# Performance work log

Hardware: AMD Instinct MI355X
Metric: run time of the kernel (lower is better)

Reference implementation:

```python
import jax, jax.numpy as jnp
import numpy as np

U = 359347   # user_num (hardcoded in source)
I = 292589   # item_num (hardcoded in source)
D = 64       # factor_num
NNZ = 4_000_000
B = 32768
LAM = 0.001  # lamada


def setup_inputs() -> dict:
    key = jax.random.key(0)
    ks = jax.random.split(key, 19)
    return {
        "ui_rows": jax.random.randint(ks[0], (NNZ,), 0, U, dtype=jnp.int32),
        "ui_cols": jax.random.randint(ks[1], (NNZ,), 0, I, dtype=jnp.int32),
        "ui_vals": jax.random.uniform(ks[2], (NNZ,), dtype=jnp.float32),
        "iu_vals": jax.random.uniform(ks[3], (NNZ,), dtype=jnp.float32),
        "d_i": jax.random.uniform(ks[4], (U,), dtype=jnp.float32),
        "d_j": jax.random.uniform(ks[5], (I,), dtype=jnp.float32),
        "embed_user": jax.random.normal(ks[6], (U, D), dtype=jnp.float32) * 0.01,
        "embed_item": jax.random.normal(ks[7], (I, D), dtype=jnp.float32) * 0.01,
        "add_w": jax.random.normal(ks[8], (1, 3), dtype=jnp.float32),
        "fw1": jax.random.normal(ks[9], (2 * D, D), dtype=jnp.float32) * (1.0 / np.sqrt(D)),
        "fb1": jax.random.normal(ks[10], (2 * D,), dtype=jnp.float32) * 0.01,
        "fw2": jax.random.normal(ks[11], (D, 2 * D), dtype=jnp.float32) * (1.0 / np.sqrt(2 * D)),
        "fb2": jax.random.normal(ks[12], (D,), dtype=jnp.float32) * 0.01,
        "user_bias": jax.random.normal(ks[13], (U, 1), dtype=jnp.float32) * 0.01,
        "item_bias": jax.random.normal(ks[14], (I, 1), dtype=jnp.float32) * 0.01,
        "avg_rating": jax.random.uniform(ks[15], (1,), dtype=jnp.float32) * 5.0,
        "user0": jax.random.randint(ks[16], (B,), 0, U, dtype=jnp.int32),
        "item_i0": jax.random.randint(ks[17], (B,), 0, I, dtype=jnp.int32),
        "ratings": jax.random.uniform(ks[18], (B,), dtype=jnp.float32) * 5.0,
    }


def _spmm(rows, cols, vals, x, num_rows):
    # sparse [num_rows, *] COO @ dense x : gather rows of x by col index,
    # scale by edge value, scatter-add into destination rows.
    return jax.ops.segment_sum(vals[:, None] * x[cols], rows, num_segments=num_rows)


def _leaky(x):
    return jnp.where(x > 0, x, 0.1 * x)


def _user_filter(x, fw1, fb1, fw2, fb2):
    h = _leaky(x @ fw1.T + fb1)
    return _leaky(h @ fw2.T + fb2)


def reference(ui_rows, ui_cols, ui_vals, iu_vals, d_i, d_j,
              embed_user, embed_item, add_w, fw1, fb1, fw2, fb2,
              user_bias, item_bias, avg_rating, user0, item_i0, ratings):
    ue, ie = embed_user, embed_item
    # layer 1: SpMM + degree-scaled residual + ReLU
    g1_u = jax.nn.relu(_spmm(ui_rows, ui_cols, ui_vals, ie, U) + ue * d_i[:, None])
    g1_i = jax.nn.relu(_spmm(ui_cols, ui_rows, iu_vals, ue, I) + ie * d_j[:, None])
    # layer 2
    g2_u = jax.nn.relu(_spmm(ui_rows, ui_cols, ui_vals, g1_i, U) + g1_u * d_i[:, None])
    g2_i = jax.nn.relu(_spmm(ui_cols, ui_rows, iu_vals, g1_u, I) + g1_i * d_j[:, None])
    # learned combination of the 3 layers: Linear(3,1) over the stacked axis
    w = add_w[0]  # [3]
    gcn_u = w[0] * ue + w[1] * g1_u + w[2] * g2_u   # [U, D]
    gcn_i = w[0] * ie + w[1] * g1_i + w[2] * g2_i   # [I, D]
    # batch lookup + shared filter MLP
    user = _user_filter(gcn_u[user0], fw1, fb1, fw2, fb2)      # [B, D]
    item = _user_filter(gcn_i[item_i0], fw1, fb1, fw2, fb2)    # [B, D]
    pred = (user * item).sum(-1) + user_bias[user0, 0] + item_bias[item_i0, 0] + avg_rating
    l2 = LAM * jnp.mean(gcn_u ** 2) + LAM * jnp.mean(gcn_i ** 2)
    loss2 = jnp.mean((pred - ratings) ** 2)
    return loss2 + l2
```

## Files before the change

kernel.cpp:

```cpp
#include <hip/hip_runtime.h>

#define U_NUM 359347
#define I_NUM 292589
#define DDIM  64
#define NNZ_N 4000000
#define BATCH 32768
#define LAM_F 0.001f
#define ACC_SLOTS 2048

#define EPB   4096
#define NBLK  ((NNZ_N + EPB - 1) / EPB)
#define NB_U  ((U_NUM + 1023) >> 10)
#define NB_I  ((I_NUM + 1023) >> 10)

__device__ __forceinline__ float leaky(float x) { return x > 0.f ? x : 0.1f * x; }

__device__ __forceinline__ unsigned short f2bf(float f) {
    unsigned b = __float_as_uint(f);
    b = (b + 0x7FFF + ((b >> 16) & 1)) >> 16;
    return (unsigned short)b;
}
__device__ __forceinline__ float bf2f(unsigned short u) {
    return __uint_as_float((unsigned)u << 16);
}
__device__ __forceinline__ float bflo(unsigned u) { return __uint_as_float(u << 16); }
__device__ __forceinline__ float bfhi(unsigned u) { return __uint_as_float(u & 0xffff0000u); }

__device__ __forceinline__ unsigned char f2fp8(float v) {
    v = fminf(fmaxf(v * 64.f, -440.f), 440.f);
    unsigned b = __float_as_uint(v * 0x1p-120f);
    unsigned sign = (b >> 24) & 0x80u;
    unsigned mag = b & 0x7fffffffu;
    mag += 0x7ffffu + ((mag >> 20) & 1u);
    return (unsigned char)(sign | ((mag >> 20) & 0x7fu));
}
#if __has_builtin(__builtin_amdgcn_cvt_f32_fp8)
#define FP8DEC(b) __builtin_amdgcn_cvt_f32_fp8((int)(b), 0)
#else
#define FP8DEC(b) (__uint_as_float(((unsigned)((b) & 0x80u) << 24) | \
                                   ((unsigned)((b) & 0x7fu) << 20)) * 0x1p120f)
#endif

__global__ __launch_bounds__(256) void f2bf8_k(
    const float4* __restrict__ inU, ushort4* __restrict__ obU, uchar4* __restrict__ o8U,
    const float4* __restrict__ inI, ushort4* __restrict__ obI, uchar4* __restrict__ o8I,
    size_t nU4, size_t total4)
{
    size_t stride = (size_t)gridDim.x * 256;
    for (size_t i = (size_t)blockIdx.x * 256 + threadIdx.x; i < total4; i += stride) {
        const float4* in; ushort4* ob; uchar4* o8; size_t j;
        if (i < nU4) { in = inU; ob = obU; o8 = o8U; j = i; }
        else         { in = inI; ob = obI; o8 = o8I; j = i - nU4; }
        float4 v = in[j];
        ushort4 o;
        o.x = f2bf(v.x); o.y = f2bf(v.y); o.z = f2bf(v.z); o.w = f2bf(v.w);
        ob[j] = o;
        uchar4 p;
        p.x = f2fp8(v.x); p.y = f2fp8(v.y); p.z = f2fp8(v.z); p.w = f2fp8(v.w);
        o8[j] = p;
    }
}

__global__ __launch_bounds__(256) void hist2_k(
    const int* __restrict__ rows, const int* __restrict__ cols,
    int* __restrict__ gh_u, int* __restrict__ gh_i)
{
    __shared__ int h[512];
    int sideB = blockIdx.x >= NBLK;
    int blk = sideB ? blockIdx.x - NBLK : blockIdx.x;
    const int* keys = sideB ? cols : rows;
    int nb = sideB ? NB_I : NB_U;
    int* gh = sideB ? gh_i : gh_u;
    for (int i = threadIdx.x; i < nb; i += 256) h[i] = 0;
    __syncthreads();
    int base = blk * EPB;
    int end = min(base + EPB, NNZ_N);
    for (int e = base + threadIdx.x; e < end; e += 256)
        atomicAdd(&h[keys[e] >> 10], 1);
    __syncthreads();
    for (int i = threadIdx.x; i < nb; i += 256)
        gh[i * NBLK + blk] = h[i];
}

__global__ __launch_bounds__(256) void scan1m_k(
    int* __restrict__ aU, int nUe, int* __restrict__ bsU, int nb1U,
    int* __restrict__ aI, int nIe, int* __restrict__ bsI)
{
    __shared__ int s[256];
    int sideB = (int)blockIdx.x >= nb1U;
    int blk = sideB ? blockIdx.x - nb1U : blockIdx.x;
    int* a = sideB ? aI : aU;
    int n = sideB ? nIe : nUe;
    int* bsum = sideB ? bsI : bsU;
    int t = threadIdx.x;
    int base = blk * 1024 + t * 4;
    int v[4];
#pragma unroll
    for (int j = 0; j < 4; ++j) v[j] = (base + j < n) ? a[base + j] : 0;
    s[t] = v[0] + v[1] + v[2] + v[3];
    __syncthreads();
    for (int off = 1; off < 256; off <<= 1) {
        int x = (t >= off) ? s[t - off] : 0;
        __syncthreads();
        s[t] += x;
        __syncthreads();
    }
    if (t == 255) bsum[blk] = s[255];
    int run = (t > 0) ? s[t - 1] : 0;
#pragma unroll
    for (int j = 0; j < 4; ++j) {
        if (base + j < n) a[base + j] = run;
        run += v[j];
    }
}

__global__ __launch_bounds__(512) void scan2m_k(
    int* __restrict__ bsU, int nbU, int* __restrict__ bsI, int nbI)
{
    __shared__ int s[512];
    int* bsum = blockIdx.x ? bsI : bsU;
    int nb = blockIdx.x ? nbI : nbU;
    int t = threadIdx.x;
    int v = (t < nb) ? bsum[t] : 0;
    s[t] = v;
    __syncthreads();
    for (int off = 1; off < 512; off <<= 1) {
        int x = (t >= off) ? s[t - off] : 0;
        __syncthreads();
        s[t] += x;
        __syncthreads();
    }
    if (t < nb) bsum[t] = s[t] - v;
}

__global__ __launch_bounds__(256) void scan3m_k(
    int* __restrict__ aU, int nUe, const int* __restrict__ bsU, int nb1U,
    int* __restrict__ aI, int nIe, const int* __restrict__ bsI)
{
    int sideB = (int)blockIdx.x >= nb1U;
    int blk = sideB ? blockIdx.x - nb1U : blockIdx.x;
    int* a = sideB ? aI : aU;
    int n = sideB ? nIe : nUe;
    int add = (sideB ? bsI : bsU)[blk];
    int base = blk * 1024 + threadIdx.x * 4;
#pragma unroll
    for (int j = 0; j < 4; ++j)
        if (base + j < n) a[base + j] += add;
}

__global__ __launch_bounds__(256) void scat_k(
    const int* __restrict__ keys, const int* __restrict__ cols,
    const float* __restrict__ vals, const int* __restrict__ gh, int nb,
    int2* __restrict__ tmpb, unsigned short* __restrict__ tmpv)
{
    __shared__ int cur[512];
    for (int i = threadIdx.x; i < nb; i += 256) cur[i] = gh[i * NBLK + blockIdx.x];
    __syncthreads();
    int base = blockIdx.x * EPB;
    int end = min(base + EPB, NNZ_N);
    for (int e = base + threadIdx.x; e < end; e += 256) {
        int k = keys[e];
        int pos = atomicAdd(&cur[k >> 10], 1);
        tmpb[pos] = make_int2(k, cols[e]);
        tmpv[pos] = f2bf(vals[e] * 0.015625f);
    }
}

__global__ __launch_bounds__(256) void l2sort_k(
    const int2* __restrict__ tmpb, const unsigned short* __restrict__ tmpv,
    const int* __restrict__ gh, int nb, int* __restrict__ ptr, int nrows,
    int* __restrict__ ecol, unsigned short* __restrict__ eval)
{
    __shared__ int hist[1024];
    __shared__ int ssc[256];
    int b = blockIdx.x;
    int t = threadIdx.x;
    int bucket_base = gh[b * NBLK];
    int bucket_end  = (b == nb - 1) ? NNZ_N : gh[(b + 1) * NBLK];
    for (int i = t; i < 1024; i += 256) hist[i] = 0;
    __syncthreads();
    for (int e = bucket_base + t; e < bucket_end; e += 256)
        atomicAdd(&hist[tmpb[e].x & 1023], 1);
    __syncthreads();
    int v0 = hist[t * 4], v1 = hist[t * 4 + 1], v2 = hist[t * 4 + 2], v3 = hist[t * 4 + 3];
    ssc[t] = v0 + v1 + v2 + v3;
    __syncthreads();
    for (int off = 1; off < 256; off <<= 1) {
        int x = (t >= off) ? ssc[t - off] : 0;
        __syncthreads();
        ssc[t] += x;
        __syncthreads();
    }
    int run = (t > 0) ? ssc[t - 1] : 0;
    int g0 = run, g1 = run + v0, g2 = g1 + v1, g3 = g2 + v2;
    hist[t * 4] = g0; hist[t * 4 + 1] = g1; hist[t * 4 + 2] = g2; hist[t * 4 + 3] = g3;
    int rbase = b << 10;
    if (rbase + t * 4 < nrows)     ptr[rbase + t * 4]     = bucket_base + g0;
    if (rbase + t * 4 + 1 < nrows) ptr[rbase + t * 4 + 1] = bucket_base + g1;
    if (rbase + t * 4 + 2 < nrows) ptr[rbase + t * 4 + 2] = bucket_base + g2;
    if (rbase + t * 4 + 3 < nrows) ptr[rbase + t * 4 + 3] = bucket_base + g3;
    if (b == nb - 1 && t == 0) ptr[nrows] = NNZ_N;
    __syncthreads();
    for (int e = bucket_base + t; e < bucket_end; e += 256) {
        int2 q = tmpb[e];
        int pos = bucket_base + atomicAdd(&hist[q.x & 1023], 1);
        ecol[pos] = q.y;
        eval[pos] = tmpv[e];
    }
}

template <int MODE>
__global__ __launch_bounds__(256) void spmm_dual_k(
    int gA,
    const int* __restrict__ ptrA, const int* __restrict__ ecolA, const unsigned short* __restrict__ evalA,
    const unsigned char* __restrict__ x8A, const unsigned short* baseA, const float* __restrict__ degA,
    unsigned short* outA, int nA, unsigned char* __restrict__ out8A,
    const unsigned short* embedA, float* __restrict__ accA,
    const int* __restrict__ ptrB, const int* __restrict__ ecolB, const unsigned short* __restrict__ evalB,
    const unsigned char* __restrict__ x8B, const unsigned short* baseB, const float* __restrict__ degB,
    unsigned short* outB, int nB, unsigned char* __restrict__ out8B,
    const unsigned short* embedB, float* __restrict__ accB,
    const float* __restrict__ add_w)
{
    int wv = threadIdx.x >> 6, lane = threadIdx.x & 63;
    int bid = blockIdx.x;
    int sideB = bid >= gA;
    int lb = sideB ? bid - gA : bid;
    const int* ptr = sideB ? ptrB : ptrA;
    const int* ecol = sideB ? ecolB : ecolA;
    const unsigned short* eval = sideB ? evalB : evalA;
    const unsigned char* x8 = sideB ? x8B : x8A;
    const unsigned short* base = sideB ? baseB : baseA;
    const float* deg = sideB ? degB : degA;
    unsigned short* out = sideB ? outB : outA;
    int nrows = sideB ? nB : nA;
    __shared__ float ssum[4];
    int r = lb * 4 + wv;
    if (r < nrows) {
        int s0 = __builtin_amdgcn_readfirstlane(ptr[r]);
        int e0 = __builtin_amdgcn_readfirstlane(ptr[r + 1]);
        float a0 = 0.f, a1 = 0.f, a2 = 0.f, a3 = 0.f;
        int k = s0;
        for (; k + 8 <= e0; k += 8) {
            int c0 = ecol[k],     c1 = ecol[k + 1], c2 = ecol[k + 2], c3 = ecol[k + 3];
            int c4 = ecol[k + 4], c5 = ecol[k + 5], c6 = ecol[k + 6], c7 = ecol[k + 7];
            unsigned char b0 = x8[(size_t)c0 * DDIM + lane];
            unsigned char b1 = x8[(size_t)c1 * DDIM + lane];
            unsigned char b2 = x8[(size_t)c2 * DDIM + lane];
            unsigned char b3 = x8[(size_t)c3 * DDIM + lane];
            unsigned char b4 = x8[(size_t)c4 * DDIM + lane];
            unsigned char b5 = x8[(size_t)c5 * DDIM + lane];
            unsigned char b6 = x8[(size_t)c6 * DDIM + lane];
            unsigned char b7 = x8[(size_t)c7 * DDIM + lane];
            a0 = fmaf(bf2f(eval[k]),     FP8DEC(b0), a0);
            a1 = fmaf(bf2f(eval[k + 1]), FP8DEC(b1), a1);
            a2 = fmaf(bf2f(eval[k + 2]), FP8DEC(b2), a2);
            a3 = fmaf(bf2f(eval[k + 3]), FP8DEC(b3), a3);
            a0 = fmaf(bf2f(eval[k + 4]), FP8DEC(b4), a0);
            a1 = fmaf(bf2f(eval[k + 5]), FP8DEC(b5), a1);
            a2 = fmaf(bf2f(eval[k + 6]), FP8DEC(b6), a2);
            a3 = fmaf(bf2f(eval[k + 7]), FP8DEC(b7), a3);
        }
        for (; k + 4 <= e0; k += 4) {
            int c0 = ecol[k], c1 = ecol[k + 1], c2 = ecol[k + 2], c3 = ecol[k + 3];
            unsigned char b0 = x8[(size_t)c0 * DDIM + lane];
            unsigned char b1 = x8[(size_t)c1 * DDIM + lane];
            unsigned char b2 = x8[(size_t)c2 * DDIM + lane];
            unsigned char b3 = x8[(size_t)c3 * DDIM + lane];
            a0 = fmaf(bf2f(eval[k]),     FP8DEC(b0), a0);
            a1 = fmaf(bf2f(eval[k + 1]), FP8DEC(b1), a1);
            a2 = fmaf(bf2f(eval[k + 2]), FP8DEC(b2), a2);
            a3 = fmaf(bf2f(eval[k + 3]), FP8DEC(b3), a3);
        }
        for (; k < e0; ++k)
            a0 = fmaf(bf2f(eval[k]), FP8DEC(x8[(size_t)ecol[k] * DDIM + lane]), a0);
        float acc = (a0 + a1) + (a2 + a3);
        float bb = bf2f(base[(size_t)r * DDIM + lane]);
        float o = fmaxf(fmaf(bb, deg[r], acc), 0.f);
        if (MODE == 0) {
            out[(size_t)r * DDIM + lane] = f2bf(o);
            (sideB ? out8B : out8A)[(size_t)r * DDIM + lane] = f2fp8(o);
        } else {
            const unsigned short* embed = sideB ? embedB : embedA;
            float g = fmaf(add_w[0], bf2f(embed[(size_t)r * DDIM + lane]),
                           fmaf(add_w[1], bb, add_w[2] * o));
            out[(size_t)r * DDIM + lane] = f2bf(g);
            float sq = g * g;
            for (int off = 32; off; off >>= 1) sq += __shfl_down(sq, off);
            if (lane == 0) ssum[wv] = sq;
        }
    } else if (MODE == 1) {
        if (lane == 0) ssum[wv] = 0.f;
    }
    if (MODE == 1) {
        __syncthreads();
        if (threadIdx.x == 0)
            atomicAdd(&(sideB ? accB : accA)[lb & (ACC_SLOTS - 1)],
                      ssum[0] + ssum[1] + ssum[2] + ssum[3]);
    }
}

__global__ __launch_bounds__(256) void mlp_k(
    const int* __restrict__ user0, const int* __restrict__ item0,
    const unsigned short* __restrict__ gcnU, const unsigned short* __restrict__ gcnI,
    const float* __restrict__ fw1, const float* __restrict__ fb1,
    const float* __restrict__ fw2, const float* __restrict__ fb2,
    unsigned short* __restrict__ ou, unsigned short* __restrict__ oi)
{
    __shared__ unsigned short xs[64][72];
    __shared__ unsigned short w1s[128][68];
    __shared__ unsigned short w2s[64][140];
    __shared__ unsigned short hs[128][72];
    __shared__ float b1s[128];
    __shared__ float b2s[64];

    int t = threadIdx.x;
    int side = blockIdx.x >> 9;
    int tile = blockIdx.x & 511;
    const int* sel = side ? item0 : user0;
    const unsigned short* gcn = side ? gcnI : gcnU;
    unsigned short* outp = side ? oi : ou;

    {
        int r = t >> 2, c = t & 3;
        int idx = sel[tile * 64 + r];
        const ushort4* src = (const ushort4*)(gcn + (size_t)idx * 64 + c * 16);
        ushort4 v0 = src[0], v1 = src[1], v2 = src[2], v3 = src[3];
        int k0 = c * 16;
        xs[k0 +  0][r] = v0.x; xs[k0 +  1][r] = v0.y; xs[k0 +  2][r] = v0.z; xs[k0 +  3][r] = v0.w;
        xs[k0 +  4][r] = v1.x; xs[k0 +  5][r] = v1.y; xs[k0 +  6][r] = v1.z; xs[k0 +  7][r] = v1.w;
        xs[k0 +  8][r] = v2.x; xs[k0 +  9][r] = v2.y; xs[k0 + 10][r] = v2.z; xs[k0 + 11][r] = v2.w;
        xs[k0 + 12][r] = v3.x; xs[k0 + 13][r] = v3.y; xs[k0 + 14][r] = v3.z; xs[k0 + 15][r] = v3.w;
    }
#pragma unroll
    for (int i = 0; i < 8; ++i) {
        int flat = i * 1024 + t * 4;
        float4 w = *(const float4*)(fw1 + flat);
        int o = flat >> 6, k = flat & 63;
        *(unsigned*)&w1s[o][k]     = (unsigned)f2bf(w.x) | ((unsigned)f2bf(w.y) << 16);
        *(unsigned*)&w1s[o][k + 2] = (unsigned)f2bf(w.z) | ((unsigned)f2bf(w.w) << 16);
        float4 u = *(const float4*)(fw2 + flat);
        int o2 = flat >> 7, k2 = flat & 127;
        *(unsigned*)&w2s[o2][k2]     = (unsigned)f2bf(u.x) | ((unsigned)f2bf(u.y) << 16);
        *(unsigned*)&w2s[o2][k2 + 2] = (unsigned)f2bf(u.z) | ((unsigned)f2bf(u.w) << 16);
    }
    if (t < 128) b1s[t] = fb1[t];
    if (t < 64)  b2s[t] = fb2[t];
    __syncthreads();

    int sg = t & 15, og = t >> 4;

    float acc[4][8];
#pragma unroll
    for (int i = 0; i < 4; ++i)
#pragma unroll
        for (int j = 0; j < 8; ++j) acc[i][j] = 0.f;

    for (int kc = 0; kc < 64; kc += 4) {
        uint2 xp0 = *(const uint2*)&xs[kc    ][sg * 4];
        uint2 xp1 = *(const uint2*)&xs[kc + 1][sg * 4];
        uint2 xp2 = *(const uint2*)&xs[kc + 2][sg * 4];
        uint2 xp3 = *(const uint2*)&xs[kc + 3][sg * 4];
        float x0[4] = { bflo(xp0.x), bfhi(xp0.x), bflo(xp0.y), bfhi(xp0.y) };
        float x1[4] = { bflo(xp1.x), bfhi(xp1.x), bflo(xp1.y), bfhi(xp1.y) };
        float x2[4] = { bflo(xp2.x), bfhi(xp2.x), bflo(xp2.y), bfhi(xp2.y) };
        float x3[4] = { bflo(xp3.x), bfhi(xp3.x), bflo(xp3.y), bfhi(xp3.y) };
#pragma unroll
        for (int j = 0; j < 8; ++j) {
            uint2 wp = *(const uint2*)&w1s[og * 8 + j][kc];
            float w0 = bflo(wp.x), w1v = bfhi(wp.x), w2v = bflo(wp.y), w3v = bfhi(wp.y);
#pragma unroll
            for (int i = 0; i < 4; ++i) {
                acc[i][j] = fmaf(x0[i], w0,  acc[i][j]);
                acc[i][j] = fmaf(x1[i], w1v, acc[i][j]);
                acc[i][j] = fmaf(x2[i], w2v, acc[i][j]);
                acc[i][j] = fmaf(x3[i], w3v, acc[i][j]);
            }
        }
    }
#pragma unroll
    for (int j = 0; j < 8; ++j) {
        int o = og * 8 + j;
        float b = b1s[o];
        float h0 = leaky(acc[0][j] + b), h1 = leaky(acc[1][j] + b);
        float h2 = leaky(acc[2][j] + b), h3 = leaky(acc[3][j] + b);
        *(unsigned*)&hs[o][sg * 4]     = (unsigned)f2bf(h0) | ((unsigned)f2bf(h1) << 16);
        *(unsigned*)&hs[o][sg * 4 + 2] = (unsigned)f2bf(h2) | ((unsigned)f2bf(h3) << 16);
    }
    __syncthreads();

    float acc2[4][4];
#pragma unroll
    for (int i = 0; i < 4; ++i)
#pragma unroll
        for (int j = 0; j < 4; ++j) acc2[i][j] = 0.f;

    for (int kc = 0; kc < 128; kc += 4) {
        uint2 hp0 = *(const uint2*)&hs[kc    ][sg * 4];
        uint2 hp1 = *(const uint2*)&hs[kc + 1][sg * 4];
        uint2 hp2 = *(const uint2*)&hs[kc + 2][sg * 4];
        uint2 hp3 = *(const uint2*)&hs[kc + 3][sg * 4];
        float h0[4] = { bflo(hp0.x), bfhi(hp0.x), bflo(hp0.y), bfhi(hp0.y) };
        float h1[4] = { bflo(hp1.x), bfhi(hp1.x), bflo(hp1.y), bfhi(hp1.y) };
        float h2[4] = { bflo(hp2.x), bfhi(hp2.x), bflo(hp2.y), bfhi(hp2.y) };
        float h3[4] = { bflo(hp3.x), bfhi(hp3.x), bflo(hp3.y), bfhi(hp3.y) };
#pragma unroll
        for (int j = 0; j < 4; ++j) {
            uint2 wp = *(const uint2*)&w2s[og * 4 + j][kc];
            float w0 = bflo(wp.x), w1v = bfhi(wp.x), w2v = bflo(wp.y), w3v = bfhi(wp.y);
#pragma unroll
            for (int i = 0; i < 4; ++i) {
                acc2[i][j] = fmaf(h0[i], w0,  acc2[i][j]);
                acc2[i][j] = fmaf(h1[i], w1v, acc2[i][j]);
                acc2[i][j] = fmaf(h2[i], w2v, acc2[i][j]);
                acc2[i][j] = fmaf(h3[i], w3v, acc2[i][j]);
            }
        }
    }
#pragma unroll
    for (int i = 0; i < 4; ++i) {
        float o0 = leaky(acc2[i][0] + b2s[og * 4 + 0]);
        float o1 = leaky(acc2[i][1] + b2s[og * 4 + 1]);
        float o2 = leaky(acc2[i][2] + b2s[og * 4 + 2]);
        float o3 = leaky(acc2[i][3] + b2s[og * 4 + 3]);
        uint2 pp;
        pp.x = (unsigned)f2bf(o0) | ((unsigned)f2bf(o1) << 16);
        pp.y = (unsigned)f2bf(o2) | ((unsigned)f2bf(o3) << 16);
        *(uint2*)(outp + ((size_t)(tile * 64 + sg * 4 + i) * 64 + og * 4)) = pp;
    }
}

__global__ __launch_bounds__(256) void dot_sse_k(
    const unsigned short* __restrict__ ou, const unsigned short* __restrict__ oi,
    const int* __restrict__ user0, const int* __restrict__ item0,
    const float* __restrict__ ub, const float* __restrict__ ib,
    const float* __restrict__ avg, const float* __restrict__ ratings,
    float* __restrict__ sse)
{
    int g = blockIdx.x * 256 + threadIdx.x;
    int b = g >> 2, q = g & 3;
    const uint4* pu = (const uint4*)(ou + (size_t)b * 64 + q * 16);
    const uint4* pi = (const uint4*)(oi + (size_t)b * 64 + q * 16);
    uint4 a0 = pu[0], a1 = pu[1];
    uint4 c0 = pi[0], c1 = pi[1];
    float s = 0.f;
#define DOTP(ua, uc) { s = fmaf(bflo(ua), bflo(uc), s); s = fmaf(bfhi(ua), bfhi(uc), s); }
    DOTP(a0.x, c0.x) DOTP(a0.y, c0.y) DOTP(a0.z, c0.z) DOTP(a0.w, c0.w)
    DOTP(a1.x, c1.x) DOTP(a1.y, c1.y) DOTP(a1.z, c1.z) DOTP(a1.w, c1.w)
#undef DOTP
    s += __shfl_xor(s, 1);
    s += __shfl_xor(s, 2);
    float contrib = 0.f;
    if (q == 0) {
        float pred = s + ub[user0[b]] + ib[item0[b]] + avg[0];
        float d = pred - ratings[b];
        contrib = d * d;
    }
    for (int off = 32; off; off >>= 1) contrib += __shfl_down(contrib, off);
    __shared__ float wsum[4];
    int lane = threadIdx.x & 63, wv = threadIdx.x >> 6;
    if (lane == 0) wsum[wv] = contrib;
    __syncthreads();
    if (threadIdx.x == 0)
        atomicAdd(sse, wsum[0] + wsum[1] + wsum[2] + wsum[3]);
}

__global__ __launch_bounds__(256) void finalize2_k(
    const float* __restrict__ accU, const float* __restrict__ accI,
    const float* __restrict__ sse, float* __restrict__ out)
{
    int t = threadIdx.x;
    float su = 0.f, si = 0.f;
    for (int i = t; i < ACC_SLOTS; i += 256) { su += accU[i]; si += accI[i]; }
    for (int off = 32; off; off >>= 1) {
        su += __shfl_down(su, off);
        si += __shfl_down(si, off);
    }
    __shared__ float s[8];
    int wv = t >> 6, lane = t & 63;
    if (lane == 0) { s[wv] = su; s[wv + 4] = si; }
    __syncthreads();
    if (t == 0) {
        float SU = s[0] + s[1] + s[2] + s[3];
        float SI = s[4] + s[5] + s[6] + s[7];
        out[0] = sse[0] / (float)BATCH
               + LAM_F * (SU / (float)((double)U_NUM * 64.0))
               + LAM_F * (SI / (float)((double)I_NUM * 64.0));
    }
}


extern "C" void kernel_launch(void* const* d_in, const int* in_sizes, int n_in,
                              void* d_out, int out_size, void* d_ws, size_t ws_size,
                              hipStream_t stream)
{
    const int*   ui_rows = (const int*)d_in[0];
    const int*   ui_cols = (const int*)d_in[1];
    const float* ui_vals = (const float*)d_in[2];
    const float* iu_vals = (const float*)d_in[3];
    const float* d_i     = (const float*)d_in[4];
    const float* d_j     = (const float*)d_in[5];
    const float* eu      = (const float*)d_in[6];
    const float* ei      = (const float*)d_in[7];
    const float* add_w   = (const float*)d_in[8];
    const float* fw1     = (const float*)d_in[9];
    const float* fb1     = (const float*)d_in[10];
    const float* fw2     = (const float*)d_in[11];
    const float* fb2     = (const float*)d_in[12];
    const float* ub      = (const float*)d_in[13];
    const float* ib      = (const float*)d_in[14];
    const float* avg     = (const float*)d_in[15];
    const int*   user0   = (const int*)d_in[16];
    const int*   item0   = (const int*)d_in[17];
    const float* ratings = (const float*)d_in[18];

    const size_t U64 = (size_t)U_NUM * DDIM;
    const size_t I64 = (size_t)I_NUM * DDIM;

    int*            ecol_u = (int*)d_ws;
    unsigned short* eval_u = (unsigned short*)(ecol_u + NNZ_N);
    int*            ecol_i = (int*)(eval_u + NNZ_N);
    unsigned short* eval_i = (unsigned short*)(ecol_i + NNZ_N);
    int2*           tmpb   = (int2*)(eval_i + NNZ_N);
    unsigned short* tmpv   = (unsigned short*)(tmpb + NNZ_N);
    unsigned char*  g1u_f8 = (unsigned char*)tmpb;
    unsigned short* ou_bf  = (unsigned short*)(g1u_f8 + ((U64 + 15) & ~15ull));
    unsigned short* oi_bf  = ou_bf + (size_t)BATCH * 64;
    int*  gh_u  = (int*)(tmpv + NNZ_N);
    int*  gh_i  = gh_u + (size_t)NB_U * NBLK;
    int*  bsumU = gh_i + (size_t)NB_I * NBLK;
    int*  bsumI = bsumU + 512;
    int*  ptr_u = bsumI + 512;
    int*  ptr_i = ptr_u + (U_NUM + 1);
    float* accU = (float*)(ptr_i + (I_NUM + 1));
    float* accI = accU + ACC_SLOTS;
    float* sse  = accI + ACC_SLOTS;
    unsigned short* eu_bf  = (unsigned short*)(sse + 4);
    unsigned short* ei_bf  = eu_bf + U64;
    unsigned short* g1u_bf = ei_bf + I64;
    unsigned short* g1i_bf = g1u_bf + U64;
    unsigned char*  eu_f8  = (unsigned char*)(g1i_bf + I64);
    unsigned char*  ei_f8  = eu_f8 + U64;
    unsigned char*  g1i_f8 = ei_f8 + I64;
    (void)ws_size;

    dim3 blk(256);
    int gu = (U_NUM + 3) / 4, gi = (I_NUM + 3) / 4;
    int nUe = NB_U * NBLK, nIe = NB_I * NBLK;
    int nb1U = (nUe + 1023) / 1024, nb1I = (nIe + 1023) / 1024;

    size_t meta_bytes = ((char*)(sse + 4)) - (char*)gh_u;
    hipMemsetAsync(gh_u, 0, meta_bytes, stream);

    f2bf8_k<<<2048, blk, 0, stream>>>((const float4*)eu, (ushort4*)eu_bf, (uchar4*)eu_f8,
                                      (const float4*)ei, (ushort4*)ei_bf, (uchar4*)ei_f8,
                                      U64 / 4, (U64 + I64) / 4);

    hist2_k<<<2 * NBLK, blk, 0, stream>>>(ui_rows, ui_cols, gh_u, gh_i);
    scan1m_k<<<nb1U + nb1I, blk, 0, stream>>>(gh_u, nUe, bsumU, nb1U, gh_i, nIe, bsumI);
    scan2m_k<<<2, 512, 0, stream>>>(bsumU, nb1U, bsumI, nb1I);
    scan3m_k<<<nb1U + nb1I, blk, 0, stream>>>(gh_u, nUe, bsumU, nb1U, gh_i, nIe, bsumI);

    scat_k<<<NBLK, blk, 0, stream>>>(ui_rows, ui_cols, ui_vals, gh_u, NB_U, tmpb, tmpv);
    l2sort_k<<<NB_U, blk, 0, stream>>>(tmpb, tmpv, gh_u, NB_U, ptr_u, U_NUM, ecol_u, eval_u);
    scat_k<<<NBLK, blk, 0, stream>>>(ui_cols, ui_rows, iu_vals, gh_i, NB_I, tmpb, tmpv);
    l2sort_k<<<NB_I, blk, 0, stream>>>(tmpb, tmpv, gh_i, NB_I, ptr_i, I_NUM, ecol_i, eval_i);

    spmm_dual_k<0><<<gu + gi, blk, 0, stream>>>(gu,
        ptr_u, ecol_u, eval_u, ei_f8, eu_bf, d_i, g1u_bf, U_NUM, g1u_f8, nullptr, nullptr,
        ptr_i, ecol_i, eval_i, eu_f8, ei_bf, d_j, g1i_bf, I_NUM, g1i_f8, nullptr, nullptr,
        nullptr);
    spmm_dual_k<1><<<gi + gu, blk, 0, stream>>>(gi,
        ptr_i, ecol_i, eval_i, g1u_f8, g1i_bf, d_j, ei_bf, I_NUM, nullptr, ei_bf, accI,
        ptr_u, ecol_u, eval_u, g1i_f8, g1u_bf, d_i, g1u_bf, U_NUM, nullptr, eu_bf, accU,
        add_w);

    mlp_k<<<1024, blk, 0, stream>>>(user0, item0, g1u_bf, ei_bf,
                                    fw1, fb1, fw2, fb2, ou_bf, oi_bf);
    dot_sse_k<<<BATCH * 4 / 256, blk, 0, stream>>>(ou_bf, oi_bf, user0, item0,
                                                   ub, ib, avg, ratings, sse);
    finalize2_k<<<1, blk, 0, stream>>>(accU, accI, sse, (float*)d_out);
}
```

Baseline: 1.228 ms.

## Drop bf16 embedding copies, pack sort keys, and merge user/item scatter-sort launches

Removes the bf16 copies of the embeddings and layer-1 outputs and reads the fp8 versions (scaled by 1/64) for the residual and layer-combination terms, which cuts conversion-kernel writes and SpMM reads. The two-pass bucket sort now packs the column and low key bits into one 32-bit word instead of an int2. It also merges the user and item scatter and local-sort kernels into single launches that use separate temp buffers. This lowers memory traffic and launch count, but the residual base and embedding terms now carry fp8 precision, which adds error to the loss.

New measurement: 1.157 ms, median of 2. 1.06x faster.

```diff
diff --git a/kernel.cpp b/kernel.cpp
--- a/kernel.cpp
+++ b/kernel.cpp
@@ -40,21 +40,19 @@
 #define FP8DEC(b) (__uint_as_float(((unsigned)((b) & 0x80u) << 24) | \
                                    ((unsigned)((b) & 0x7fu) << 20)) * 0x1p120f)
 #endif
-
-__global__ __launch_bounds__(256) void f2bf8_k(
-    const float4* __restrict__ inU, ushort4* __restrict__ obU, uchar4* __restrict__ o8U,
-    const float4* __restrict__ inI, ushort4* __restrict__ obI, uchar4* __restrict__ o8I,
+#define INV64 0.015625f
+
+__global__ __launch_bounds__(256) void f2f8_k(
+    const float4* __restrict__ inU, uchar4* __restrict__ o8U,
+    const float4* __restrict__ inI, uchar4* __restrict__ o8I,
     size_t nU4, size_t total4)
 {
     size_t stride = (size_t)gridDim.x * 256;
     for (size_t i = (size_t)blockIdx.x * 256 + threadIdx.x; i < total4; i += stride) {
-        const float4* in; ushort4* ob; uchar4* o8; size_t j;
-        if (i < nU4) { in = inU; ob = obU; o8 = o8U; j = i; }
-        else         { in = inI; ob = obI; o8 = o8I; j = i - nU4; }
+        const float4* in; uchar4* o8; size_t j;
+        if (i < nU4) { in = inU; o8 = o8U; j = i; }
+        else         { in = inI; o8 = o8I; j = i - nU4; }
         float4 v = in[j];
-        ushort4 o;
-        o.x = f2bf(v.x); o.y = f2bf(v.y); o.z = f2bf(v.z); o.w = f2bf(v.w);
-        ob[j] = o;
         uchar4 p;
         p.x = f2fp8(v.x); p.y = f2fp8(v.y); p.z = f2fp8(v.z); p.w = f2fp8(v.w);
         o8[j] = p;
@@ -148,39 +146,62 @@
         if (base + j < n) a[base + j] += add;
 }
 
-__global__ __launch_bounds__(256) void scat_k(
-    const int* __restrict__ keys, const int* __restrict__ cols,
-    const float* __restrict__ vals, const int* __restrict__ gh, int nb,
-    int2* __restrict__ tmpb, unsigned short* __restrict__ tmpv)
+__global__ __launch_bounds__(256) void scat2_k(
+    const int* __restrict__ rows, const int* __restrict__ cols,
+    const float* __restrict__ uv, const float* __restrict__ iv,
+    const int* __restrict__ gh_u, const int* __restrict__ gh_i,
+    unsigned* __restrict__ tc_u, unsigned short* __restrict__ tv_u,
+    unsigned* __restrict__ tc_i, unsigned short* __restrict__ tv_i)
 {
     __shared__ int cur[512];
-    for (int i = threadIdx.x; i < nb; i += 256) cur[i] = gh[i * NBLK + blockIdx.x];
-    __syncthreads();
-    int base = blockIdx.x * EPB;
+    int sideB = blockIdx.x >= NBLK;
+    int blk = sideB ? blockIdx.x - NBLK : blockIdx.x;
+    const int* keys = sideB ? cols : rows;
+    const int* other = sideB ? rows : cols;
+    const float* vals = sideB ? iv : uv;
+    const int* gh = sideB ? gh_i : gh_u;
+    int nb = sideB ? NB_I : NB_U;
+    unsigned* tc = sideB ? tc_i : tc_u;
+    unsigned short* tv = sideB ? tv_i : tv_u;
+    for (int i = threadIdx.x; i < nb; i += 256) cur[i] = gh[i * NBLK + blk];
+    __syncthreads();
+    int base = blk * EPB;
     int end = min(base + EPB, NNZ_N);
     for (int e = base + threadIdx.x; e < end; e += 256) {
         int k = keys[e];
         int pos = atomicAdd(&cur[k >> 10], 1);
-        tmpb[pos] = make_int2(k, cols[e]);
-        tmpv[pos] = f2bf(vals[e] * 0.015625f);
-    }
-}
-
-__global__ __launch_bounds__(256) void l2sort_k(
-    const int2* __restrict__ tmpb, const unsigned short* __restrict__ tmpv,
-    const int* __restrict__ gh, int nb, int* __restrict__ ptr, int nrows,
-    int* __restrict__ ecol, unsigned short* __restrict__ eval)
+        tc[pos] = ((unsigned)other[e] << 10) | (unsigned)(k & 1023);
+        tv[pos] = f2bf(vals[e] * INV64);
+    }
+}
+
+__global__ __launch_bounds__(256) void l2sort2_k(
+    const unsigned* __restrict__ tc_u, const unsigned short* __restrict__ tv_u,
+    const unsigned* __restrict__ tc_i, const unsigned short* __restrict__ tv_i,
+    const int* __restrict__ gh_u, const int* __restrict__ gh_i,
+    int* __restrict__ ptr_u, int* __restrict__ ptr_i,
+    int* __restrict__ ecol_u, unsigned short* __restrict__ eval_u,
+    int* __restrict__ ecol_i, unsigned short* __restrict__ eval_i)
 {
     __shared__ int hist[1024];
     __shared__ int ssc[256];
-    int b = blockIdx.x;
+    int sideB = blockIdx.x >= NB_U;
+    int b = sideB ? blockIdx.x - NB_U : blockIdx.x;
+    const unsigned* tc = sideB ? tc_i : tc_u;
+    const unsigned short* tv = sideB ? tv_i : tv_u;
+    const int* gh = sideB ? gh_i : gh_u;
+    int nb = sideB ? NB_I : NB_U;
+    int nrows = sideB ? I_NUM : U_NUM;
+    int* ptr = sideB ? ptr_i : ptr_u;
+    int* ecol = sideB ? ecol_i : ecol_u;
+    unsigned short* eval = sideB ? eval_i : eval_u;
     int t = threadIdx.x;
     int bucket_base = gh[b * NBLK];
     int bucket_end  = (b == nb - 1) ? NNZ_N : gh[(b + 1) * NBLK];
     for (int i = t; i < 1024; i += 256) hist[i] = 0;
     __syncthreads();
     for (int e = bucket_base + t; e < bucket_end; e += 256)
-        atomicAdd(&hist[tmpb[e].x & 1023], 1);
+        atomicAdd(&hist[tc[e] & 1023u], 1);
     __syncthreads();
     int v0 = hist[t * 4], v1 = hist[t * 4 + 1], v2 = hist[t * 4 + 2], v3 = hist[t * 4 + 3];
     ssc[t] = v0 + v1 + v2 + v3;
@@ -202,10 +223,10 @@
     if (b == nb - 1 && t == 0) ptr[nrows] = NNZ_N;
     __syncthreads();
     for (int e = bucket_base + t; e < bucket_end; e += 256) {
-        int2 q = tmpb[e];
-        int pos = bucket_base + atomicAdd(&hist[q.x & 1023], 1);
-        ecol[pos] = q.y;
-        eval[pos] = tmpv[e];
+        unsigned q = tc[e];
+        int pos = bucket_base + atomicAdd(&hist[q & 1023u], 1);
+        ecol[pos] = (int)(q >> 10);
+        eval[pos] = tv[e];
     }
 }
 
@@ -213,13 +234,15 @@
 __global__ __launch_bounds__(256) void spmm_dual_k(
     int gA,
     const int* __restrict__ ptrA, const int* __restrict__ ecolA, const unsigned short* __restrict__ evalA,
-    const unsigned char* __restrict__ x8A, const unsigned short* baseA, const float* __restrict__ degA,
-    unsigned short* outA, int nA, unsigned char* __restrict__ out8A,
-    const unsigned short* embedA, float* __restrict__ accA,
+    const unsigned char* __restrict__ x8A, const unsigned char* __restrict__ base8A,
+    const float* __restrict__ degA, int nA,
+    unsigned char* __restrict__ out8A, unsigned short* __restrict__ outbA,
+    const unsigned char* __restrict__ emb8A, float* __restrict__ accA,
     const int* __restrict__ ptrB, const int* __restrict__ ecolB, const unsigned short* __restrict__ evalB,
-    const unsigned char* __restrict__ x8B, const unsigned short* baseB, const float* __restrict__ degB,
-    unsigned short* outB, int nB, unsigned char* __restrict__ out8B,
-    const unsigned short* embedB, float* __restrict__ accB,
+    const unsigned char* __restrict__ x8B, const unsigned char* __restrict__ base8B,
+    const float* __restrict__ degB, int nB,
+    unsigned char* __restrict__ out8B, unsigned short* __restrict__ outbB,
+    const unsigned char* __restrict__ emb8B, float* __restrict__ accB,
     const float* __restrict__ add_w)
 {
     int wv = threadIdx.x >> 6, lane = threadIdx.x & 63;
@@ -230,9 +253,8 @@
     const int* ecol = sideB ? ecolB : ecolA;
     const unsigned short* eval = sideB ? evalB : evalA;
     const unsigned char* x8 = sideB ? x8B : x8A;
-    const unsigned short* base = sideB ? baseB : baseA;
+    const unsigned char* base8 = sideB ? base8B : base8A;
     const float* deg = sideB ? degB : degA;
-    unsigned short* out = sideB ? outB : outA;
     int nrows = sideB ? nB : nA;
     __shared__ float ssum[4];
     int r = lb * 4 + wv;
@@ -275,16 +297,16 @@
         for (; k < e0; ++k)
             a0 = fmaf(bf2f(eval[k]), FP8DEC(x8[(size_t)ecol[k] * DDIM + lane]), a0);
         float acc = (a0 + a1) + (a2 + a3);
-        float bb = bf2f(base[(size_t)r * DDIM + lane]);
-        float o = fmaxf(fmaf(bb, deg[r], acc), 0.f);
+        float bb64 = FP8DEC(base8[(size_t)r * DDIM + lane]);
+        float o = fmaxf(fmaf(bb64, deg[r] * INV64, acc), 0.f);
         if (MODE == 0) {
-            out[(size_t)r * DDIM + lane] = f2bf(o);
             (sideB ? out8B : out8A)[(size_t)r * DDIM + lane] = f2fp8(o);
         } else {
-            const unsigned short* embed = sideB ? embedB : embedA;
-            float g = fmaf(add_w[0], bf2f(embed[(size_t)r * DDIM + lane]),
-                           fmaf(add_w[1], bb, add_w[2] * o));
-            out[(size_t)r * DDIM + lane] = f2bf(g);
+            const unsigned char* emb8 = sideB ? emb8B : emb8A;
+            float e64 = FP8DEC(emb8[(size_t)r * DDIM + lane]);
+            float g = fmaf(add_w[0] * INV64, e64,
+                      fmaf(add_w[1] * INV64, bb64, add_w[2] * o));
+            (sideB ? outbB : outbA)[(size_t)r * DDIM + lane] = f2bf(g);
             float sq = g * g;
             for (int off = 32; off; off >>= 1) sq += __shfl_down(sq, off);
             if (lane == 0) ssum[wv] = sq;
@@ -521,12 +543,15 @@
     unsigned short* eval_u = (unsigned short*)(ecol_u + NNZ_N);
     int*            ecol_i = (int*)(eval_u + NNZ_N);
     unsigned short* eval_i = (unsigned short*)(ecol_i + NNZ_N);
-    int2*           tmpb   = (int2*)(eval_i + NNZ_N);
-    unsigned short* tmpv   = (unsigned short*)(tmpb + NNZ_N);
-    unsigned char*  g1u_f8 = (unsigned char*)tmpb;
-    unsigned short* ou_bf  = (unsigned short*)(g1u_f8 + ((U64 + 15) & ~15ull));
+    unsigned short* ou_bf  = (unsigned short*)ecol_u;
     unsigned short* oi_bf  = ou_bf + (size_t)BATCH * 64;
-    int*  gh_u  = (int*)(tmpv + NNZ_N);
+    unsigned*       tc_u   = (unsigned*)(eval_i + NNZ_N);
+    unsigned short* tv_u   = (unsigned short*)(tc_u + NNZ_N);
+    unsigned*       tc_i   = (unsigned*)(tv_u + NNZ_N);
+    unsigned short* tv_i   = (unsigned short*)(tc_i + NNZ_N);
+    unsigned char*  g1u_f8 = (unsigned char*)tc_u;
+    unsigned char*  g1i_f8 = g1u_f8 + ((U64 + 15) & ~15ull);
+    int*  gh_u  = (int*)(tv_i + NNZ_N);
     int*  gh_i  = gh_u + (size_t)NB_U * NBLK;
     int*  bsumU = gh_i + (size_t)NB_I * NBLK;
     int*  bsumI = bsumU + 512;
@@ -535,13 +560,10 @@
     float* accU = (float*)(ptr_i + (I_NUM + 1));
     float* accI = accU + ACC_SLOTS;
     float* sse  = accI + ACC_SLOTS;
-    unsigned short* eu_bf  = (unsigned short*)(sse + 4);
-    unsigned short* ei_bf  = eu_bf + U64;
-    unsigned short* g1u_bf = ei_bf + I64;
-    unsigned short* g1i_bf = g1u_bf + U64;
-    unsigned char*  eu_f8  = (unsigned char*)(g1i_bf + I64);
-    unsigned char*  ei_f8  = eu_f8 + U64;
-    unsigned char*  g1i_f8 = ei_f8 + I64;
+    unsigned char*  eu_f8  = (unsigned char*)(sse + 4);
+    unsigned char*  ei_f8  = eu_f8 + ((U64 + 15) & ~15ull);
+    unsigned short* gcnU_bf = (unsigned short*)(ei_f8 + ((I64 + 15) & ~15ull));
+    unsigned short* gcnI_bf = gcnU_bf + U64;
     (void)ws_size;
 
     dim3 blk(256);
@@ -552,30 +574,30 @@
     size_t meta_bytes = ((char*)(sse + 4)) - (char*)gh_u;
     hipMemsetAsync(gh_u, 0, meta_bytes, stream);
 
-    f2bf8_k<<<2048, blk, 0, stream>>>((const float4*)eu, (ushort4*)eu_bf, (uchar4*)eu_f8,
-                                      (const float4*)ei, (ushort4*)ei_bf, (uchar4*)ei_f8,
-                                      U64 / 4, (U64 + I64) / 4);
+    f2f8_k<<<2048, blk, 0, stream>>>((const float4*)eu, (uchar4*)eu_f8,
+                                     (const float4*)ei, (uchar4*)ei_f8,
+                                     U64 / 4, (U64 + I64) / 4);
 
     hist2_k<<<2 * NBLK, blk, 0, stream>>>(ui_rows, ui_cols, gh_u, gh_i);
     scan1m_k<<<nb1U + nb1I, blk, 0, stream>>>(gh_u, nUe, bsumU, nb1U, gh_i, nIe, bsumI);
     scan2m_k<<<2, 512, 0, stream>>>(bsumU, nb1U, bsumI, nb1I);
     scan3m_k<<<nb1U + nb1I, blk, 0, stream>>>(gh_u, nUe, bsumU, nb1U, gh_i, nIe, bsumI);
 
-    scat_k<<<NBLK, blk, 0, stream>>>(ui_rows, ui_cols, ui_vals, gh_u, NB_U, tmpb, tmpv);
-    l2sort_k<<<NB_U, blk, 0, stream>>>(tmpb, tmpv, gh_u, NB_U, ptr_u, U_NUM, ecol_u, eval_u);
-    scat_k<<<NBLK, blk, 0, stream>>>(ui_cols, ui_rows, iu_vals, gh_i, NB_I, tmpb, tmpv);
-    l2sort_k<<<NB_I, blk, 0, stream>>>(tmpb, tmpv, gh_i, NB_I, ptr_i, I_NUM, ecol_i, eval_i);
+    scat2_k<<<2 * NBLK, blk, 0, stream>>>(ui_rows, ui_cols, ui_vals, iu_vals,
+                                          gh_u, gh_i, tc_u, tv_u, tc_i, tv_i);
+    l2sort2_k<<<NB_U + NB_I, blk, 0, stream>>>(tc_u, tv_u, tc_i, tv_i, gh_u, gh_i,
+                                               ptr_u, ptr_i, ecol_u, eval_u, ecol_i, eval_i);
 
     spmm_dual_k<0><<<gu + gi, blk, 0, stream>>>(gu,
-        ptr_u, ecol_u, eval_u, ei_f8, eu_bf, d_i, g1u_bf, U_NUM, g1u_f8, nullptr, nullptr,
-        ptr_i, ecol_i, eval_i, eu_f8, ei_bf, d_j, g1i_bf, I_NUM, g1i_f8, nullptr, nullptr,
+        ptr_u, ecol_u, eval_u, ei_f8, eu_f8, d_i, U_NUM, g1u_f8, nullptr, nullptr, nullptr,
+        ptr_i, ecol_i, eval_i, eu_f8, ei_f8, d_j, I_NUM, g1i_f8, nullptr, nullptr, nullptr,
         nullptr);
     spmm_dual_k<1><<<gi + gu, blk, 0, stream>>>(gi,
-        ptr_i, ecol_i, eval_i, g1u_f8, g1i_bf, d_j, ei_bf, I_NUM, nullptr, ei_bf, accI,
-        ptr_u, ecol_u, eval_u, g1i_f8, g1u_bf, d_i, g1u_bf, U_NUM, nullptr, eu_bf, accU,
+        ptr_i, ecol_i, eval_i, g1u_f8, g1i_f8, d_j, I_NUM, nullptr, gcnI_bf, ei_f8, accI,
+        ptr_u, ecol_u, eval_u, g1i_f8, g1u_f8, d_i, U_NUM, nullptr, gcnU_bf, eu_f8, accU,
         add_w);
 
-    mlp_k<<<1024, blk, 0, stream>>>(user0, item0, g1u_bf, ei_bf,
+    mlp_k<<<1024, blk, 0, stream>>>(user0, item0, gcnU_bf, gcnI_bf,
                                     fw1, fb1, fw2, fb2, ou_bf, oi_bf);
     dot_sse_k<<<BATCH * 4 / 256, blk, 0, stream>>>(ou_bf, oi_bf, user0, item0,
                                                    ub, ib, avg, ratings, sse);
```
